# Optimization experiments

Hardware: AMD Instinct MI355X
Metric: run time of the kernel (lower is better)

## Reference

```python
import jax, jax.numpy as jnp
import numpy as np

DIM_IN = 25
H = 128        # num_neurons
P = 8000       # num_pixel
BS = 32
NEG_SLOPE = 0.01  # torch LeakyReLU default


def _leaky(x):
    return jnp.where(x >= 0, x, NEG_SLOPE * x)


def setup_inputs() -> dict:
    key = jax.random.key(0)
    ks = jax.random.split(key, 7)
    x = jax.random.normal(ks[0], (BS, DIM_IN), dtype=jnp.float32)
    # Stacked per-pixel MLP params (kaiming-ish scale to keep values sane)
    W1 = jax.random.normal(ks[1], (P, DIM_IN, H), dtype=jnp.float32) / np.sqrt(DIM_IN)
    b1 = jax.random.normal(ks[2], (P, H), dtype=jnp.float32) * 0.01
    W2 = jax.random.normal(ks[3], (P, H, H), dtype=jnp.float32) / np.sqrt(H)
    b2 = jax.random.normal(ks[4], (P, H), dtype=jnp.float32) * 0.01
    W3 = jax.random.normal(ks[5], (P, H), dtype=jnp.float32) / np.sqrt(H)
    b3 = jax.random.normal(ks[6], (P,), dtype=jnp.float32) * 0.01
    return {"x": x, "W1": W1, "b1": b1, "W2": W2, "b2": b2, "W3": W3, "b3": b3}


def reference(x, W1, b1, W2, b2, W3, b3):
    # h1: [bs, P, H] -- every pixel MLP sees the same x
    h1 = _leaky(jnp.einsum('bd,pdh->bph', x, W1) + b1[None])
    h2 = _leaky(jnp.einsum('bph,phk->bpk', h1, W2) + b2[None])
    # final Linear(num_neurons, 1) -> scalar per pixel -> y[bs, P]
    y = jnp.einsum('bph,ph->bp', h2, W3) + b3[None]
    return y
```

## Files before the change

kernel.cpp:

```cpp
#include <hip/hip_runtime.h>


constexpr int DIM_IN = 25;
constexpr int H      = 128;
constexpr int P      = 8000;
constexpr int BS     = 32;
constexpr float NEG  = 0.01f;

typedef short  short4v __attribute__((ext_vector_type(4)));
typedef short  short8v __attribute__((ext_vector_type(8)));
typedef float  f32x16  __attribute__((ext_vector_type(16)));

__device__ __forceinline__ float leaky(float v) { return v >= 0.f ? v : NEG * v; }

__device__ __forceinline__ short bf_rne(float f) {
    unsigned u = __builtin_bit_cast(unsigned, f);
    return (short)((u + 0x7fffu + ((u >> 16) & 1u)) >> 16);
}
__device__ __forceinline__ short bf_rna(float f) {
    unsigned u = __builtin_bit_cast(unsigned, f);
    return (short)((u + 0x8000u) >> 16);
}

#define STAGE_W1(BUF, T8) {                                                    \
    const float* g_ = W1p + (size_t)(8 * (T8)) * H + (t << 2);                 \
    float* d_ = &w12t[BUF][0];                                                 \
    _Pragma("unroll")                                                          \
    for (int i_ = 0; i_ < 4; ++i_)                                             \
        __builtin_amdgcn_global_load_lds(                                      \
            (const __attribute__((address_space(1))) unsigned*)(g_ + i_ * 256),\
            (__attribute__((address_space(3))) unsigned*)(d_ + i_ * 256),      \
            16, 0, 0); }

#define STAGE_T(BUF, KT, HF) {                                                 \
    const float* g_ = W2p + (size_t)(16 * (KT) + (t >> 4)) * H                 \
                      + 64 * (HF) + ((t & 15) << 2);                           \
    float* d_ = &w12t[BUF][0];                                                 \
    _Pragma("unroll")                                                          \
    for (int i_ = 0; i_ < 4; ++i_)                                             \
        __builtin_amdgcn_global_load_lds(                                      \
            (const __attribute__((address_space(1))) unsigned*)(g_ + (size_t)i_ * 4 * H), \
            (__attribute__((address_space(3))) unsigned*)(d_ + i_ * 256),      \
            16, 0, 0); }

#define L1_CONSUME(BUF, T8) {                                                  \
    _Pragma("unroll")                                                          \
    for (int dd_ = 0; dd_ < 8; ++dd_) {                                        \
        const int d_ = 8 * (T8) + dd_;                                         \
        const float4 a0_ = *reinterpret_cast<const float4*>(&sxT[d_][r0]);     \
        const float4 a1_ = *reinterpret_cast<const float4*>(&sxT[d_][r0 + 4]); \
        const float4 wl_ = *reinterpret_cast<const float4*>(&w12t[BUF][dd_ * H + c0]); \
        const float4 wh_ = *reinterpret_cast<const float4*>(&w12t[BUF][dd_ * H + 64 + c0]); \
        const float av_[8] = {a0_.x, a0_.y, a0_.z, a0_.w, a1_.x, a1_.y, a1_.z, a1_.w}; \
        const float wv_[8] = {wl_.x, wl_.y, wl_.z, wl_.w, wh_.x, wh_.y, wh_.z, wh_.w}; \
        _Pragma("unroll")                                                      \
        for (int i_ = 0; i_ < 8; ++i_)                                         \
            _Pragma("unroll")                                                  \
            for (int c_ = 0; c_ < 8; ++c_)                                     \
                aL1[i_][c_] += av_[i_] * wv_[c_];                              \
    } }

#define CONSUME_T(BUF, KT, HF) {                                               \
    const int ao_ = lo * 256 + 32 * (KT) + 16 * hi;                            \
    const short8v a_ = *reinterpret_cast<const short8v*>(                      \
        (const char*)h1b + (ao_ ^ ((lo & 7) << 4)));                           \
    const float* tb_ = &w12t[BUF][hi * 512 + lo];                              \
    _Pragma("unroll")                                                          \
    for (int n2_ = 0; n2_ < 2; ++n2_) {                                        \
        const float* col_ = tb_ + 32 * n2_;                                    \
        short8v bf_;                                                           \
        bf_[0] = bf_rna(col_[0]);   bf_[1] = bf_rna(col_[64]);                 \
        bf_[2] = bf_rna(col_[128]); bf_[3] = bf_rna(col_[192]);                \
        bf_[4] = bf_rna(col_[256]); bf_[5] = bf_rna(col_[320]);                \
        bf_[6] = bf_rna(col_[384]); bf_[7] = bf_rna(col_[448]);                \
        acc[2 * (HF) + n2_] = __builtin_amdgcn_mfma_f32_32x32x16_bf16(         \
            a_, bf_, acc[2 * (HF) + n2_], 0, 0, 0);                            \
    } }

__global__ __launch_bounds__(64, 2) void pixel_mlp_kernel(
    const float* __restrict__ x,
    const float* __restrict__ W1,
    const float* __restrict__ b1,
    const float* __restrict__ W2,
    const float* __restrict__ b2,
    const float* __restrict__ W3,
    const float* __restrict__ b3,
    float* __restrict__ y)
{
    const int p  = blockIdx.x;
    const int t  = threadIdx.x;
    const int cc = t & 15;
    const int gg = t >> 4;
    const int c0 = cc << 2;
    const int r0 = gg << 3;
    const int lo = t & 31;
    const int hi = t >> 5;

    __shared__ float sxT[DIM_IN][BS];
    __shared__ short h1b[BS][H];
    __shared__ float w12t[2][16 * 64];

    const float* W1p = W1 + (size_t)p * (DIM_IN * H);
    const float* W2p = W2 + (size_t)p * (H * H);

    const float4 b1l  = *reinterpret_cast<const float4*>(b1 + (size_t)p * H + c0);
    const float4 b1h  = *reinterpret_cast<const float4*>(b1 + (size_t)p * H + 64 + c0);
    const float4 w24l = *reinterpret_cast<const float4*>(W1p + 24 * H + c0);
    const float4 w24h = *reinterpret_cast<const float4*>(W1p + 24 * H + 64 + c0);
    float b2v[4], w3v[4];
    #pragma unroll
    for (int nb = 0; nb < 4; ++nb) {
        b2v[nb] = b2[(size_t)p * H + 32 * nb + lo];
        w3v[nb] = W3[(size_t)p * H + 32 * nb + lo];
    }
    const float b3s = b3[p];
    asm volatile("" ::: "memory");

    STAGE_W1(0, 0)
    STAGE_W1(1, 1)
    asm volatile("" ::: "memory");

    for (int i = t; i < DIM_IN * BS; i += 64)
        sxT[i >> 5][i & 31] = x[(i & 31) * DIM_IN + (i >> 5)];
    asm volatile("s_waitcnt lgkmcnt(0)" ::: "memory");

    float aL1[8][8];
    {
        const float bv[8] = {b1l.x, b1l.y, b1l.z, b1l.w, b1h.x, b1h.y, b1h.z, b1h.w};
        #pragma unroll
        for (int i = 0; i < 8; ++i)
            #pragma unroll
            for (int c = 0; c < 8; ++c)
                aL1[i][c] = bv[c];
    }

    asm volatile("s_waitcnt vmcnt(4)" ::: "memory");
    L1_CONSUME(0, 0)
    asm volatile("s_waitcnt lgkmcnt(0)" ::: "memory");
    STAGE_W1(0, 2)
    asm volatile("s_waitcnt vmcnt(4)" ::: "memory");
    L1_CONSUME(1, 1)
    asm volatile("s_waitcnt lgkmcnt(0)" ::: "memory");
    STAGE_T(1, 0, 0)
    asm volatile("s_waitcnt vmcnt(4)" ::: "memory");
    L1_CONSUME(0, 2)
    {
        const float4 a0 = *reinterpret_cast<const float4*>(&sxT[24][r0]);
        const float4 a1 = *reinterpret_cast<const float4*>(&sxT[24][r0 + 4]);
        const float av[8] = {a0.x, a0.y, a0.z, a0.w, a1.x, a1.y, a1.z, a1.w};
        const float wv[8] = {w24l.x, w24l.y, w24l.z, w24l.w,
                             w24h.x, w24h.y, w24h.z, w24h.w};
        #pragma unroll
        for (int i = 0; i < 8; ++i)
            #pragma unroll
            for (int c = 0; c < 8; ++c)
                aL1[i][c] += av[i] * wv[c];
    }
    asm volatile("s_waitcnt lgkmcnt(0)" ::: "memory");
    STAGE_T(0, 0, 1)

    #pragma unroll
    for (int i = 0; i < 8; ++i) {
        short4v lov, hiv;
        lov[0] = bf_rne(leaky(aL1[i][0])); lov[1] = bf_rne(leaky(aL1[i][1]));
        lov[2] = bf_rne(leaky(aL1[i][2])); lov[3] = bf_rne(leaky(aL1[i][3]));
        hiv[0] = bf_rne(leaky(aL1[i][4])); hiv[1] = bf_rne(leaky(aL1[i][5]));
        hiv[2] = bf_rne(leaky(aL1[i][6])); hiv[3] = bf_rne(leaky(aL1[i][7]));
        const int ro = (r0 + i) * 256;
        const int sz = ((r0 + i) & 7) << 4;
        *reinterpret_cast<short4v*>((char*)h1b + ((ro + 8 * cc) ^ sz))       = lov;
        *reinterpret_cast<short4v*>((char*)h1b + ((ro + 128 + 8 * cc) ^ sz)) = hiv;
    }
    asm volatile("s_waitcnt lgkmcnt(0)" ::: "memory");
    __builtin_amdgcn_sched_barrier(0);

    f32x16 acc[4];
    #pragma unroll
    for (int nb = 0; nb < 4; ++nb)
        acc[nb] = (f32x16)(0.f);

    #pragma unroll 1
    for (int kt = 0; kt < 7; ++kt) {
        asm volatile("s_waitcnt vmcnt(4)" ::: "memory");
        CONSUME_T(1, kt, 0)
        asm volatile("s_waitcnt lgkmcnt(0)" ::: "memory");
        STAGE_T(1, kt + 1, 0)
        asm volatile("s_waitcnt vmcnt(4)" ::: "memory");
        CONSUME_T(0, kt, 1)
        asm volatile("s_waitcnt lgkmcnt(0)" ::: "memory");
        STAGE_T(0, kt + 1, 1)
    }
    asm volatile("s_waitcnt vmcnt(4)" ::: "memory");
    CONSUME_T(1, 7, 0)
    asm volatile("s_waitcnt vmcnt(0)" ::: "memory");
    CONSUME_T(0, 7, 1)

    float s[16];
    #pragma unroll
    for (int reg = 0; reg < 16; ++reg) {
        float acc_s = 0.f;
        #pragma unroll
        for (int nb = 0; nb < 4; ++nb)
            acc_s += leaky(acc[nb][reg] + b2v[nb]) * w3v[nb];
        s[reg] = acc_s;
    }
    #pragma unroll
    for (int m = 16; m >= 1; m >>= 1) {
        #pragma unroll
        for (int reg = 0; reg < 16; ++reg)
            s[reg] += __shfl_xor(s[reg], m);
    }
    if (lo == 0) {
        #pragma unroll
        for (int reg = 0; reg < 16; ++reg) {
            const int r = (reg & 3) + 8 * (reg >> 2) + 4 * hi;
            y[(size_t)r * P + p] = s[reg] + b3s;
        }
    }
}

extern "C" void kernel_launch(void* const* d_in, const int* in_sizes, int n_in,
                              void* d_out, int out_size, void* d_ws, size_t ws_size,
                              hipStream_t stream) {
    const float* x  = (const float*)d_in[0];
    const float* W1 = (const float*)d_in[1];
    const float* b1 = (const float*)d_in[2];
    const float* W2 = (const float*)d_in[3];
    const float* b2 = (const float*)d_in[4];
    const float* W3 = (const float*)d_in[5];
    const float* b3 = (const float*)d_in[6];
    float* y = (float*)d_out;

    pixel_mlp_kernel<<<dim3(P), dim3(64), 0, stream>>>(x, W1, b1, W2, b2, W3, b3, y);
}
```

Measured before the change: 131.4 us.

## Process four pixels per block with cross-pixel prefetch of next weights

Each block now handles four consecutive pixels instead of one, launching a quarter as many blocks. While finishing the last layer-2 tile of one pixel, it prefetches the next pixel's W1 tiles and small bias/W3 vectors, hiding the pipeline fill latency between pixels. This removes per-block prologue cost (x transpose, initial load stalls) at the price of fewer blocks (2000) for occupancy and larger code. Buffer roles alternate per pixel to keep the double buffer consistent.

```diff
diff --git a/kernel.cpp b/kernel.cpp
--- a/kernel.cpp
+++ b/kernel.cpp
@@ -5,6 +5,8 @@
 constexpr int H      = 128;
 constexpr int P      = 8000;
 constexpr int BS     = 32;
+constexpr int NPIX   = 4;
+constexpr int GRID   = P / NPIX;
 constexpr float NEG  = 0.01f;
 
 typedef short  short4v __attribute__((ext_vector_type(4)));
@@ -22,8 +24,8 @@
     return (short)((u + 0x8000u) >> 16);
 }
 
-#define STAGE_W1(BUF, T8) {                                                    \
-    const float* g_ = W1p + (size_t)(8 * (T8)) * H + (t << 2);                 \
+#define STAGE_W1P(BUF, T8, W1Q) {                                              \
+    const float* g_ = (W1Q) + (size_t)(8 * (T8)) * H + (t << 2);               \
     float* d_ = &w12t[BUF][0];                                                 \
     _Pragma("unroll")                                                          \
     for (int i_ = 0; i_ < 4; ++i_)                                             \
@@ -32,8 +34,8 @@
             (__attribute__((address_space(3))) unsigned*)(d_ + i_ * 256),      \
             16, 0, 0); }
 
-#define STAGE_T(BUF, KT, HF) {                                                 \
-    const float* g_ = W2p + (size_t)(16 * (KT) + (t >> 4)) * H                 \
+#define STAGE_TP(BUF, KT, HF, W2Q) {                                           \
+    const float* g_ = (W2Q) + (size_t)(16 * (KT) + (t >> 4)) * H               \
                       + 64 * (HF) + ((t & 15) << 2);                           \
     float* d_ = &w12t[BUF][0];                                                 \
     _Pragma("unroll")                                                          \
@@ -77,6 +79,137 @@
             a_, bf_, acc[2 * (HF) + n2_], 0, 0, 0);                            \
     } }
 
+#define LOAD_SMALLS(PP) {                                                      \
+    const float* W1q_ = W1 + (size_t)(PP) * (DIM_IN * H);                      \
+    nb1l  = *reinterpret_cast<const float4*>(b1 + (size_t)(PP) * H + c0);      \
+    nb1h  = *reinterpret_cast<const float4*>(b1 + (size_t)(PP) * H + 64 + c0); \
+    nw24l = *reinterpret_cast<const float4*>(W1q_ + 24 * H + c0);              \
+    nw24h = *reinterpret_cast<const float4*>(W1q_ + 24 * H + 64 + c0);         \
+    _Pragma("unroll")                                                          \
+    for (int q_ = 0; q_ < 4; ++q_) {                                           \
+        nb2v[q_] = b2[(size_t)(PP) * H + 32 * q_ + lo];                        \
+        nw3v[q_] = W3[(size_t)(PP) * H + 32 * q_ + lo];                        \
+    }                                                                          \
+    nb3 = b3[PP]; }
+
+#define PIX_HEAD(A, B, PCUR)                                                   \
+    const float4 b1l = nb1l, b1h = nb1h, w24l = nw24l, w24h = nw24h;           \
+    float b2v[4], w3v[4];                                                      \
+    _Pragma("unroll")                                                          \
+    for (int q_ = 0; q_ < 4; ++q_) { b2v[q_] = nb2v[q_]; w3v[q_] = nw3v[q_]; } \
+    const float b3s = nb3;                                                     \
+    const float* W1p = W1 + (size_t)(PCUR) * (DIM_IN * H);                     \
+    const float* W2p = W2 + (size_t)(PCUR) * (H * H);                          \
+    float aL1[8][8];                                                           \
+    {                                                                          \
+        const float bv[8] = {b1l.x, b1l.y, b1l.z, b1l.w,                       \
+                             b1h.x, b1h.y, b1h.z, b1h.w};                      \
+        _Pragma("unroll")                                                      \
+        for (int i_ = 0; i_ < 8; ++i_)                                         \
+            _Pragma("unroll")                                                  \
+            for (int c_ = 0; c_ < 8; ++c_)                                     \
+                aL1[i_][c_] = bv[c_];                                          \
+    }                                                                          \
+    asm volatile("s_waitcnt vmcnt(4)" ::: "memory");       \
+    L1_CONSUME(A, 0)                                                           \
+    asm volatile("s_waitcnt lgkmcnt(0)" ::: "memory");                         \
+    STAGE_W1P(A, 2, W1p)                                                       \
+    asm volatile("s_waitcnt vmcnt(4)" ::: "memory");              \
+    L1_CONSUME(B, 1)                                                           \
+    asm volatile("s_waitcnt lgkmcnt(0)" ::: "memory");                         \
+    STAGE_TP(B, 0, 0, W2p)                                                     \
+    asm volatile("s_waitcnt vmcnt(4)" ::: "memory");              \
+    L1_CONSUME(A, 2)                                                           \
+    {                                    \
+        const float4 a0 = *reinterpret_cast<const float4*>(&sxT[24][r0]);      \
+        const float4 a1 = *reinterpret_cast<const float4*>(&sxT[24][r0 + 4]);  \
+        const float av[8] = {a0.x, a0.y, a0.z, a0.w, a1.x, a1.y, a1.z, a1.w};  \
+        const float wv[8] = {w24l.x, w24l.y, w24l.z, w24l.w,                   \
+                             w24h.x, w24h.y, w24h.z, w24h.w};                  \
+        _Pragma("unroll")                                                      \
+        for (int i_ = 0; i_ < 8; ++i_)                                         \
+            _Pragma("unroll")                                                  \
+            for (int c_ = 0; c_ < 8; ++c_)                                     \
+                aL1[i_][c_] += av[i_] * wv[c_];                                \
+    }                                                                          \
+    asm volatile("s_waitcnt lgkmcnt(0)" ::: "memory");                         \
+    STAGE_TP(A, 0, 1, W2p)                                                     \
+    _Pragma("unroll")                                                          \
+    for (int i_ = 0; i_ < 8; ++i_) {               \
+        short4v lov, hiv;                                                      \
+        lov[0] = bf_rne(leaky(aL1[i_][0])); lov[1] = bf_rne(leaky(aL1[i_][1]));\
+        lov[2] = bf_rne(leaky(aL1[i_][2])); lov[3] = bf_rne(leaky(aL1[i_][3]));\
+        hiv[0] = bf_rne(leaky(aL1[i_][4])); hiv[1] = bf_rne(leaky(aL1[i_][5]));\
+        hiv[2] = bf_rne(leaky(aL1[i_][6])); hiv[3] = bf_rne(leaky(aL1[i_][7]));\
+        const int ro_ = (r0 + i_) * 256;                                       \
+        const int sz_ = ((r0 + i_) & 7) << 4;                                  \
+        *reinterpret_cast<short4v*>((char*)h1b + ((ro_ + 8 * cc) ^ sz_))       = lov; \
+        *reinterpret_cast<short4v*>((char*)h1b + ((ro_ + 128 + 8 * cc) ^ sz_)) = hiv; \
+    }                                                                          \
+    asm volatile("s_waitcnt lgkmcnt(0)" ::: "memory");                         \
+    __builtin_amdgcn_sched_barrier(0);                                         \
+    f32x16 acc[4];                                                             \
+    _Pragma("unroll")                                                          \
+    for (int q_ = 0; q_ < 4; ++q_) acc[q_] = (f32x16)(0.f);                    \
+    _Pragma("unroll 1")                                                        \
+    for (int kt = 0; kt < 7; ++kt) {                                           \
+        asm volatile("s_waitcnt vmcnt(4)" ::: "memory");                       \
+        CONSUME_T(B, kt, 0)                                                    \
+        asm volatile("s_waitcnt lgkmcnt(0)" ::: "memory");                     \
+        STAGE_TP(B, kt + 1, 0, W2p)                                            \
+        asm volatile("s_waitcnt vmcnt(4)" ::: "memory");                       \
+        CONSUME_T(A, kt, 1)                                                    \
+        asm volatile("s_waitcnt lgkmcnt(0)" ::: "memory");                     \
+        STAGE_TP(A, kt + 1, 1, W2p)                                            \
+    }                                                                          \
+    asm volatile("s_waitcnt vmcnt(4)" ::: "memory");                           \
+    CONSUME_T(B, 7, 0)
+
+#define LAYER3(PCUR) {                                                         \
+    float s_[16];                                                              \
+    _Pragma("unroll")                                                          \
+    for (int rg_ = 0; rg_ < 16; ++rg_) {                                       \
+        float a_ = 0.f;                                                        \
+        _Pragma("unroll")                                                      \
+        for (int q_ = 0; q_ < 4; ++q_)                                         \
+            a_ += leaky(acc[q_][rg_] + b2v[q_]) * w3v[q_];                     \
+        s_[rg_] = a_;                                                          \
+    }                                                                          \
+    _Pragma("unroll")                                                          \
+    for (int m_ = 16; m_ >= 1; m_ >>= 1) {                                     \
+        _Pragma("unroll")                                                      \
+        for (int rg_ = 0; rg_ < 16; ++rg_)                                     \
+            s_[rg_] += __shfl_xor(s_[rg_], m_);                                \
+    }                                                                          \
+    if (lo == 0) {                                                             \
+        _Pragma("unroll")                                                      \
+        for (int rg_ = 0; rg_ < 16; ++rg_) {                                   \
+            const int r_ = (rg_ & 3) + 8 * (rg_ >> 2) + 4 * hi;                \
+            y[(size_t)r_ * P + (PCUR)] = s_[rg_] + b3s;                        \
+        }                                                                      \
+    } }
+
+#define PIX_FULL(A, B, PCUR, PNEXT) {                                          \
+    PIX_HEAD(A, B, PCUR)                                                       \
+    asm volatile("s_waitcnt lgkmcnt(0)" ::: "memory");                         \
+    const float* W1n = W1 + (size_t)(PNEXT) * (DIM_IN * H);                    \
+    STAGE_W1P(B, 0, W1n)                                                       \
+    asm volatile("s_waitcnt vmcnt(4)" ::: "memory");          \
+    CONSUME_T(A, 7, 1)                                                         \
+    asm volatile("s_waitcnt lgkmcnt(0)" ::: "memory");                         \
+    LOAD_SMALLS(PNEXT)                                                         \
+    asm volatile("" ::: "memory");                                             \
+    STAGE_W1P(A, 1, W1n)                                                       \
+    LAYER3(PCUR)                                                               \
+    }
+
+#define PIX_LAST(A, B, PCUR) {                                                 \
+    PIX_HEAD(A, B, PCUR)                                                       \
+    asm volatile("s_waitcnt vmcnt(0)" ::: "memory");                           \
+    CONSUME_T(A, 7, 1)                                                         \
+    LAYER3(PCUR)                                                               \
+    }
+
 __global__ __launch_bounds__(64, 2) void pixel_mlp_kernel(
     const float* __restrict__ x,
     const float* __restrict__ W1,
@@ -87,7 +220,7 @@
     const float* __restrict__ b3,
     float* __restrict__ y)
 {
-    const int p  = blockIdx.x;
+    const int p0 = blockIdx.x * NPIX;
     const int t  = threadIdx.x;
     const int cc = t & 15;
     const int gg = t >> 4;
@@ -100,123 +233,25 @@
     __shared__ short h1b[BS][H];
     __shared__ float w12t[2][16 * 64];
 
-    const float* W1p = W1 + (size_t)p * (DIM_IN * H);
-    const float* W2p = W2 + (size_t)p * (H * H);
-
-    const float4 b1l  = *reinterpret_cast<const float4*>(b1 + (size_t)p * H + c0);
-    const float4 b1h  = *reinterpret_cast<const float4*>(b1 + (size_t)p * H + 64 + c0);
-    const float4 w24l = *reinterpret_cast<const float4*>(W1p + 24 * H + c0);
-    const float4 w24h = *reinterpret_cast<const float4*>(W1p + 24 * H + 64 + c0);
-    float b2v[4], w3v[4];
-    #pragma unroll
-    for (int nb = 0; nb < 4; ++nb) {
-        b2v[nb] = b2[(size_t)p * H + 32 * nb + lo];
-        w3v[nb] = W3[(size_t)p * H + 32 * nb + lo];
-    }
-    const float b3s = b3[p];
-    asm volatile("" ::: "memory");
-
-    STAGE_W1(0, 0)
-    STAGE_W1(1, 1)
-    asm volatile("" ::: "memory");
+    float4 nb1l, nb1h, nw24l, nw24h;
+    float  nb2v[4], nw3v[4], nb3;
 
     for (int i = t; i < DIM_IN * BS; i += 64)
         sxT[i >> 5][i & 31] = x[(i & 31) * DIM_IN + (i >> 5)];
-    asm volatile("s_waitcnt lgkmcnt(0)" ::: "memory");
-
-    float aL1[8][8];
+    asm volatile("s_waitcnt vmcnt(0) lgkmcnt(0)" ::: "memory");
+
+    LOAD_SMALLS(p0)
+    asm volatile("" ::: "memory");
     {
-        const float bv[8] = {b1l.x, b1l.y, b1l.z, b1l.w, b1h.x, b1h.y, b1h.z, b1h.w};
-        #pragma unroll
-        for (int i = 0; i < 8; ++i)
-            #pragma unroll
-            for (int c = 0; c < 8; ++c)
-                aL1[i][c] = bv[c];
+        const float* W1q = W1 + (size_t)p0 * (DIM_IN * H);
+        STAGE_W1P(0, 0, W1q)
+        STAGE_W1P(1, 1, W1q)
     }
 
-    asm volatile("s_waitcnt vmcnt(4)" ::: "memory");
-    L1_CONSUME(0, 0)
-    asm volatile("s_waitcnt lgkmcnt(0)" ::: "memory");
-    STAGE_W1(0, 2)
-    asm volatile("s_waitcnt vmcnt(4)" ::: "memory");
-    L1_CONSUME(1, 1)
-    asm volatile("s_waitcnt lgkmcnt(0)" ::: "memory");
-    STAGE_T(1, 0, 0)
-    asm volatile("s_waitcnt vmcnt(4)" ::: "memory");
-    L1_CONSUME(0, 2)
-    {
-        const float4 a0 = *reinterpret_cast<const float4*>(&sxT[24][r0]);
-        const float4 a1 = *reinterpret_cast<const float4*>(&sxT[24][r0 + 4]);
-        const float av[8] = {a0.x, a0.y, a0.z, a0.w, a1.x, a1.y, a1.z, a1.w};
-        const float wv[8] = {w24l.x, w24l.y, w24l.z, w24l.w,
-                             w24h.x, w24h.y, w24h.z, w24h.w};
-        #pragma unroll
-        for (int i = 0; i < 8; ++i)
-            #pragma unroll
-            for (int c = 0; c < 8; ++c)
-                aL1[i][c] += av[i] * wv[c];
-    }
-    asm volatile("s_waitcnt lgkmcnt(0)" ::: "memory");
-    STAGE_T(0, 0, 1)
-
-    #pragma unroll
-    for (int i = 0; i < 8; ++i) {
-        short4v lov, hiv;
-        lov[0] = bf_rne(leaky(aL1[i][0])); lov[1] = bf_rne(leaky(aL1[i][1]));
-        lov[2] = bf_rne(leaky(aL1[i][2])); lov[3] = bf_rne(leaky(aL1[i][3]));
-        hiv[0] = bf_rne(leaky(aL1[i][4])); hiv[1] = bf_rne(leaky(aL1[i][5]));
-        hiv[2] = bf_rne(leaky(aL1[i][6])); hiv[3] = bf_rne(leaky(aL1[i][7]));
-        const int ro = (r0 + i) * 256;
-        const int sz = ((r0 + i) & 7) << 4;
-        *reinterpret_cast<short4v*>((char*)h1b + ((ro + 8 * cc) ^ sz))       = lov;
-        *reinterpret_cast<short4v*>((char*)h1b + ((ro + 128 + 8 * cc) ^ sz)) = hiv;
-    }
-    asm volatile("s_waitcnt lgkmcnt(0)" ::: "memory");
-    __builtin_amdgcn_sched_barrier(0);
-
-    f32x16 acc[4];
-    #pragma unroll
-    for (int nb = 0; nb < 4; ++nb)
-        acc[nb] = (f32x16)(0.f);
-
-    #pragma unroll 1
-    for (int kt = 0; kt < 7; ++kt) {
-        asm volatile("s_waitcnt vmcnt(4)" ::: "memory");
-        CONSUME_T(1, kt, 0)
-        asm volatile("s_waitcnt lgkmcnt(0)" ::: "memory");
-        STAGE_T(1, kt + 1, 0)
-        asm volatile("s_waitcnt vmcnt(4)" ::: "memory");
-        CONSUME_T(0, kt, 1)
-        asm volatile("s_waitcnt lgkmcnt(0)" ::: "memory");
-        STAGE_T(0, kt + 1, 1)
-    }
-    asm volatile("s_waitcnt vmcnt(4)" ::: "memory");
-    CONSUME_T(1, 7, 0)
-    asm volatile("s_waitcnt vmcnt(0)" ::: "memory");
-    CONSUME_T(0, 7, 1)
-
-    float s[16];
-    #pragma unroll
-    for (int reg = 0; reg < 16; ++reg) {
-        float acc_s = 0.f;
-        #pragma unroll
-        for (int nb = 0; nb < 4; ++nb)
-            acc_s += leaky(acc[nb][reg] + b2v[nb]) * w3v[nb];
-        s[reg] = acc_s;
-    }
-    #pragma unroll
-    for (int m = 16; m >= 1; m >>= 1) {
-        #pragma unroll
-        for (int reg = 0; reg < 16; ++reg)
-            s[reg] += __shfl_xor(s[reg], m);
-    }
-    if (lo == 0) {
-        #pragma unroll
-        for (int reg = 0; reg < 16; ++reg) {
-            const int r = (reg & 3) + 8 * (reg >> 2) + 4 * hi;
-            y[(size_t)r * P + p] = s[reg] + b3s;
-        }
-    }
+    PIX_FULL(0, 1, p0,     p0 + 1)
+    PIX_FULL(1, 0, p0 + 1, p0 + 2)
+    PIX_FULL(0, 1, p0 + 2, p0 + 3)
+    PIX_LAST(1, 0, p0 + 3)
 }
 
 extern "C" void kernel_launch(void* const* d_in, const int* in_sizes, int n_in,
@@ -231,5 +266,5 @@
     const float* b3 = (const float*)d_in[6];
     float* y = (float*)d_out;
 
-    pixel_mlp_kernel<<<dim3(P), dim3(64), 0, stream>>>(x, W1, b1, W2, b2, W3, b3, y);
-}
+    pixel_mlp_kernel<<<dim3(GRID), dim3(64), 0, stream>>>(x, W1, b1, W2, b2, W3, b3, y);
+}
```

Measured after the change: 136.7 us. 1.04x slower.
